# Optimization experiments

Hardware: AMD Instinct MI355X
Metric: run time of the kernel (lower is better)

The kernel has to match this reference:

```python
import jax, jax.numpy as jnp
import numpy as np

C_M, C_Z, H, C = 256, 128, 8, 32  # msa emb, pair emb, heads, head channels
S, R = 128, 256                   # MSA rows, residues


def layer_norm(x, gamma, beta, eps=1e-5):
    mu = jnp.mean(x, axis=-1, keepdims=True)
    var = jnp.var(x, axis=-1, keepdims=True)
    return (x - mu) * jax.lax.rsqrt(var + eps) * gamma + beta


def setup_inputs() -> dict:
    key = jax.random.key(0)
    ks = jax.random.split(key, 12)
    sc_m = 1.0 / np.sqrt(C_M)
    sc_z = 1.0 / np.sqrt(C_Z)
    sc_hc = 1.0 / np.sqrt(H * C)
    return {
        "msa_rep": jax.random.normal(ks[0], (S, R, C_M), dtype=jnp.float32),
        "pair_rep": jax.random.normal(ks[1], (R, R, C_Z), dtype=jnp.float32),
        "ln_msa_g": jnp.ones((C_M,), jnp.float32),
        "ln_msa_b": jnp.zeros((C_M,), jnp.float32),
        "ln_pair_g": jnp.ones((C_Z,), jnp.float32),
        "ln_pair_b": jnp.zeros((C_Z,), jnp.float32),
        "w_q": jax.random.normal(ks[2], (C_M, H, C), jnp.float32) * sc_m,
        "w_k": jax.random.normal(ks[3], (C_M, H, C), jnp.float32) * sc_m,
        "w_v": jax.random.normal(ks[4], (C_M, H, C), jnp.float32) * sc_m,
        "w_g": jax.random.normal(ks[5], (C_M, H, C), jnp.float32) * sc_m,
        "b_g": jnp.zeros((H, C), jnp.float32),
        "w_b": jax.random.normal(ks[6], (C_Z, H), jnp.float32) * sc_z,
        "b_b": jnp.zeros((H,), jnp.float32),
        "w_o": jax.random.normal(ks[7], (H, C, C_M), jnp.float32) * sc_hc,
        "b_o": jnp.zeros((C_M,), jnp.float32),
    }


def reference(msa_rep, pair_rep, ln_msa_g, ln_msa_b, ln_pair_g, ln_pair_b,
              w_q, w_k, w_v, w_g, b_g, w_b, b_b, w_o, b_o):
    m = layer_norm(msa_rep, ln_msa_g, ln_msa_b)                 # [S,R,C_M]
    q = jnp.einsum('src,chd->srhd', m, w_q)                     # [S,R,H,C]
    k = jnp.einsum('src,chd->srhd', m, w_k)
    v = jnp.einsum('src,chd->srhd', m, w_v)
    gates = jax.nn.sigmoid(jnp.einsum('src,chd->srhd', m, w_g) + b_g)
    # pair bias: [R,R,H] -> [H,R,R]
    z = layer_norm(pair_rep, ln_pair_g, ln_pair_b)
    b = jnp.einsum('ijc,ch->hij', z, w_b) + b_b[:, None, None]  # [H,R,R]
    logits = jnp.einsum('sqhd,skhd->shqk', q, k) / np.sqrt(C)   # [S,H,R,R]
    logits = logits + b[None]
    w = jax.nn.softmax(logits, axis=-1)
    o = jnp.einsum('shqk,skhd->sqhd', w, v)                     # [S,R,H,C]
    o = gates * o
    out = jnp.einsum('srhd,hdc->src', o, w_o) + b_o             # [S,R,C_M]
    return out
```

## Files before the change

### kernel.cpp

```cpp
#include <hip/hip_runtime.h>
#include <hip/hip_bf16.h>

#define S_DIM 128
#define R_DIM 256
#define CM 256
#define CZ 128
#define H_DIM 8
#define C_DIM 32

typedef short bf16x8 __attribute__((ext_vector_type(8)));
typedef float f32x4 __attribute__((ext_vector_type(4)));

__device__ inline ushort f2b(float f) {
  __hip_bfloat16 b = __float2bfloat16(f);
  return *(ushort*)&b;
}
__device__ inline float b2f(ushort u) {
  __hip_bfloat16 b = *(__hip_bfloat16*)&u;
  return __bfloat162float(b);
}

#define LOG2E 1.4426950408889634f

__device__ __forceinline__ void gld_lds16(const ushort* g, ushort* l) {
  __builtin_amdgcn_global_load_lds(
      (const __attribute__((address_space(1))) unsigned int*)g,
      (__attribute__((address_space(3))) unsigned int*)l, 16, 0, 0);
}

__global__ __launch_bounds__(256) void prologue_kernel(
    const float* __restrict__ msa, const float* __restrict__ ln_msa_g,
    const float* __restrict__ ln_msa_b, ushort* __restrict__ m,
    const float* __restrict__ pair, const float* __restrict__ ln_pr_g,
    const float* __restrict__ ln_pr_b, const float* __restrict__ w_b,
    const float* __restrict__ b_b, float* __restrict__ bias,
    const float* __restrict__ wq, const float* __restrict__ wk,
    const float* __restrict__ wv, const float* __restrict__ wg,
    const float* __restrict__ wo, ushort* __restrict__ Wt5) {
  __shared__ float t[64][65];
  __shared__ float wbs[CZ][8];
  __shared__ float gs[CZ], bs[CZ];
  int b = blockIdx.x;
  int tid = threadIdx.x;
  if (b < 8192) {
    int lane = tid & 63, w = tid >> 6;
    int row = b * 4 + w;
    const float* xp = msa + (size_t)row * CM + lane * 4;
    float4 v = *(const float4*)xp;
    float s1 = v.x + v.y + v.z + v.w;
    float s2 = v.x * v.x + v.y * v.y + v.z * v.z + v.w * v.w;
#pragma unroll
    for (int off = 32; off; off >>= 1) {
      s1 += __shfl_xor(s1, off, 64);
      s2 += __shfl_xor(s2, off, 64);
    }
    float mean = s1 * (1.0f / CM);
    float rstd = rsqrtf(s2 * (1.0f / CM) - mean * mean + 1e-5f);
    float4 gv = *(const float4*)(ln_msa_g + lane * 4);
    float4 bv = *(const float4*)(ln_msa_b + lane * 4);
    ushort4 o;
    o.x = f2b((v.x - mean) * rstd * gv.x + bv.x);
    o.y = f2b((v.y - mean) * rstd * gv.y + bv.y);
    o.z = f2b((v.z - mean) * rstd * gv.z + bv.z);
    o.w = f2b((v.w - mean) * rstd * gv.w + bv.w);
    *(ushort4*)(m + (size_t)row * CM + lane * 4) = o;
  } else if (b < 9216) {
    int bb = b - 8192;
    if (tid < CZ) { gs[tid] = ln_pr_g[tid]; bs[tid] = ln_pr_b[tid]; }
    for (int i = tid; i < CZ * 8; i += 256) wbs[i >> 3][i & 7] = w_b[i];
    __syncthreads();
    int q = tid & 3;
    int row = bb * 64 + (tid >> 2);
    const float* zp = pair + (size_t)row * CZ + q * 32;
    float4 v[8];
#pragma unroll
    for (int j = 0; j < 8; ++j) v[j] = *(const float4*)(zp + j * 4);
    float s1 = 0.f, s2 = 0.f;
#pragma unroll
    for (int j = 0; j < 8; ++j) {
      s1 += v[j].x + v[j].y + v[j].z + v[j].w;
      s2 += v[j].x * v[j].x + v[j].y * v[j].y + v[j].z * v[j].z +
            v[j].w * v[j].w;
    }
    s1 += __shfl_xor(s1, 1, 64);
    s2 += __shfl_xor(s2, 1, 64);
    s1 += __shfl_xor(s1, 2, 64);
    s2 += __shfl_xor(s2, 2, 64);
    float mean = s1 * (1.0f / CZ);
    float var = s2 * (1.0f / CZ) - mean * mean;
    float rstd = rsqrtf(var + 1e-5f);
    float acc[8] = {};
#pragma unroll
    for (int j = 0; j < 8; ++j) {
      float e[4] = {v[j].x, v[j].y, v[j].z, v[j].w};
#pragma unroll
      for (int u = 0; u < 4; ++u) {
        int c = q * 32 + j * 4 + u;
        float zn = (e[u] - mean) * rstd * gs[c] + bs[c];
#pragma unroll
        for (int h = 0; h < 8; ++h) acc[h] += zn * wbs[c][h];
      }
    }
#pragma unroll
    for (int h = 0; h < 8; ++h) {
      acc[h] += __shfl_xor(acc[h], 1, 64);
      acc[h] += __shfl_xor(acc[h], 2, 64);
    }
    int h0 = q * 2;
    bias[(size_t)h0 * (R_DIM * R_DIM) + row] = (acc[h0] + b_b[h0]) * LOG2E;
    bias[(size_t)(h0 + 1) * (R_DIM * R_DIM) + row] =
        (acc[h0 + 1] + b_b[h0 + 1]) * LOG2E;
  } else {
    int zz = b - 9216;
    int z = zz >> 4, rem = zz & 15;
    int by = rem >> 2, bx = rem & 3;
    const float* W = (z == 0) ? wq : (z == 1) ? wk : (z == 2) ? wv
                     : (z == 3) ? wg : wo;
    ushort* Wt = Wt5 + (size_t)z * 65536;
    int r = tid >> 2, c4 = (tid & 3) * 16;
    int rowBase = by * 64, colBase = bx * 64;
#pragma unroll
    for (int j = 0; j < 16; ++j)
      t[r][c4 + j] = W[(size_t)(rowBase + r) * 256 + colBase + c4 + j];
    __syncthreads();
#pragma unroll
    for (int j = 0; j < 16; ++j)
      Wt[(size_t)(colBase + r) * 256 + rowBase + c4 + j] = f2b(t[c4 + j][r]);
  }
}

__global__ __launch_bounds__(512) void proj_mfma(
    const ushort* __restrict__ M, const ushort* __restrict__ Wt5,
    const float* __restrict__ b_g, ushort* __restrict__ qb,
    ushort* __restrict__ kb2, ushort* __restrict__ vb,
    ushort* __restrict__ gb) {
  __shared__ ushort As[128 * 64];
  __shared__ ushort Bs[128 * 64];
  int tid = threadIdx.x, lane = tid & 63, wid = tid >> 6;
  int lr = lane & 15, lg = lane >> 4;
  int rowBase = blockIdx.x * 128;
  int cby = blockIdx.y;
  int proj = cby >> 1;
  int sc = (lane & 7) ^ ((lane >> 3) & 7);
  const ushort* Ag =
      M + (size_t)(rowBase + wid * 8 + (lane >> 3)) * 256 + sc * 8;
  const ushort* Bg =
      Wt5 + (size_t)(cby * 128 + wid * 8 + (lane >> 3)) * 256 + sc * 8;
  int ldsrow = wid * 8 * 64;
  int wr = wid >> 2, wc = wid & 3;
  int sx = (lr & 7) * 8;
  f32x4 zf = {0.f, 0.f, 0.f, 0.f};
  f32x4 acc[4][2];
#pragma unroll
  for (int i = 0; i < 4; ++i)
#pragma unroll
    for (int j = 0; j < 2; ++j) acc[i][j] = zf;

  for (int kb = 0; kb < 4; ++kb) {
    if (kb) __syncthreads();
    gld_lds16(Ag + kb * 64, As + ldsrow);
    gld_lds16(Ag + kb * 64 + 64 * 256, As + 64 * 64 + ldsrow);
    gld_lds16(Bg + kb * 64, Bs + ldsrow);
    gld_lds16(Bg + kb * 64 + 64 * 256, Bs + 64 * 64 + ldsrow);
    __syncthreads();
#pragma unroll
    for (int kk = 0; kk < 2; ++kk) {
      bf16x8 a[4], b[2];
#pragma unroll
      for (int mf = 0; mf < 4; ++mf)
        a[mf] = *(const bf16x8*)&As[(wr * 64 + mf * 16 + lr) * 64 +
                                    ((kk * 32 + lg * 8) ^ sx)];
#pragma unroll
      for (int nf = 0; nf < 2; ++nf)
        b[nf] = *(const bf16x8*)&Bs[(wc * 32 + nf * 16 + lr) * 64 +
                                    ((kk * 32 + lg * 8) ^ sx)];
#pragma unroll
      for (int mf = 0; mf < 4; ++mf)
#pragma unroll
        for (int nf = 0; nf < 2; ++nf)
          acc[mf][nf] = __builtin_amdgcn_mfma_f32_16x16x32_bf16(
              b[nf], a[mf], acc[mf][nf], 0, 0, 0);
    }
  }
#pragma unroll
  for (int mf = 0; mf < 4; ++mf) {
    int row = rowBase + wr * 64 + mf * 16 + lr;
    int s = row >> 8, rr = row & 255;
#pragma unroll
    for (int nf = 0; nf < 2; ++nf) {
      int colL = (cby & 1) * 128 + wc * 32 + nf * 16 + lg * 4;
      int h = colL >> 5, d0 = colL & 31;
      size_t oidx = ((size_t)((s * H_DIM + h) * R_DIM + rr)) * C_DIM + d0;
      f32x4 v4 = acc[mf][nf];
      ushort4 o4;
      if (proj == 0) {
        const float qs = 0.17677669529663687f * LOG2E;
        o4.x = f2b(v4[0] * qs);
        o4.y = f2b(v4[1] * qs);
        o4.z = f2b(v4[2] * qs);
        o4.w = f2b(v4[3] * qs);
        *(ushort4*)(qb + oidx) = o4;
      } else if (proj == 1) {
        o4.x = f2b(v4[0]); o4.y = f2b(v4[1]);
        o4.z = f2b(v4[2]); o4.w = f2b(v4[3]);
        *(ushort4*)(kb2 + oidx) = o4;
      } else if (proj == 2) {
        o4.x = f2b(v4[0]); o4.y = f2b(v4[1]);
        o4.z = f2b(v4[2]); o4.w = f2b(v4[3]);
        *(ushort4*)(vb + oidx) = o4;
      } else {
        float4 bg4 = *(const float4*)(b_g + colL);
        o4.x = f2b(1.f / (1.f + __expf(-(v4[0] + bg4.x))));
        o4.y = f2b(1.f / (1.f + __expf(-(v4[1] + bg4.y))));
        o4.z = f2b(1.f / (1.f + __expf(-(v4[2] + bg4.z))));
        o4.w = f2b(1.f / (1.f + __expf(-(v4[3] + bg4.w))));
        *(ushort4*)(gb + oidx) = o4;
      }
    }
  }
}

__global__ __launch_bounds__(512, 4) void attn_mfma(
    const ushort* __restrict__ q, const ushort* __restrict__ k,
    const ushort* __restrict__ v, const ushort* __restrict__ g,
    const float* __restrict__ bias, ushort* __restrict__ ob) {
  __shared__ ushort Vt[32][260];
  __shared__ ushort Pl[8][32][66];
  int blk = blockIdx.x;
  int s = blk >> 3, h = blk & 7;
  int tid = threadIdx.x, lane = tid & 63, w = tid >> 6;
  int lr = lane & 15, lg = lane >> 4;
  size_t base = (size_t)(s * H_DIM + h) * (R_DIM * C_DIM);

  {
    int key = tid >> 1, half = (tid & 1) * 16;
    const ushort* vp = v + base + (size_t)key * 32 + half;
    bf16x8 t0 = *(const bf16x8*)vp;
    bf16x8 t1 = *(const bf16x8*)(vp + 8);
#pragma unroll
    for (int j = 0; j < 8; ++j) {
      Vt[half + j][key] = (ushort)t0[j];
      Vt[half + 8 + j][key] = (ushort)t1[j];
    }
  }
  __syncthreads();

  int qrow0 = w * 32;
  bf16x8 qf[2];
#pragma unroll
  for (int mf = 0; mf < 2; ++mf)
    qf[mf] = *(const bf16x8*)(q + base + (size_t)(qrow0 + mf * 16 + lr) * 32 +
                              lg * 8);
  const float* bp0 = bias + ((size_t)h * R_DIM + qrow0 + lg * 4) * R_DIM +
                     lr * 4;

  float lsum[2][4] = {};
  f32x4 of[2][2];
  f32x4 zf = {0.f, 0.f, 0.f, 0.f};
#pragma unroll
  for (int mf = 0; mf < 2; ++mf) {
    of[mf][0] = zf;
    of[mf][1] = zf;
  }

  bf16x8 kf[4];
#pragma unroll
  for (int nf = 0; nf < 4; ++nf)
    kf[nf] = *(const bf16x8*)(k + base + (size_t)(lr * 4 + nf) * 32 + lg * 8);

#pragma unroll
  for (int t = 0; t < 4; ++t) {
    int k0 = t * 64;
    bf16x8 kfn[4];
    if (t < 3) {
#pragma unroll
      for (int nf = 0; nf < 4; ++nf)
        kfn[nf] = *(const bf16x8*)(k + base +
                                   (size_t)(k0 + 64 + lr * 4 + nf) * 32 +
                                   lg * 8);
    }
    f32x4 sf[2][4];
    __builtin_amdgcn_s_setprio(1);
#pragma unroll
    for (int mf = 0; mf < 2; ++mf)
#pragma unroll
      for (int nf = 0; nf < 4; ++nf)
        sf[mf][nf] =
            __builtin_amdgcn_mfma_f32_16x16x32_bf16(qf[mf], kf[nf], zf, 0, 0, 0);
    __builtin_amdgcn_s_setprio(0);
#pragma unroll
    for (int mf = 0; mf < 2; ++mf) {
      float4 bv[4];
#pragma unroll
      for (int r = 0; r < 4; ++r)
        bv[r] = *(const float4*)(bp0 + (size_t)(mf * 16 + r) * R_DIM + k0);
#pragma unroll
      for (int r = 0; r < 4; ++r) {
        float p0 = __builtin_amdgcn_exp2f(sf[mf][0][r] + bv[r].x);
        float p1 = __builtin_amdgcn_exp2f(sf[mf][1][r] + bv[r].y);
        float p2 = __builtin_amdgcn_exp2f(sf[mf][2][r] + bv[r].z);
        float p3 = __builtin_amdgcn_exp2f(sf[mf][3][r] + bv[r].w);
        lsum[mf][r] += (p0 + p1) + (p2 + p3);
        ushort4 pk;
        pk.x = f2b(p0);
        pk.y = f2b(p1);
        pk.z = f2b(p2);
        pk.w = f2b(p3);
        *(ushort4*)&Pl[w][mf * 16 + lg * 4 + r][lr * 4] = pk;
      }
    }
    __builtin_amdgcn_s_setprio(1);
#pragma unroll
    for (int kt = 0; kt < 2; ++kt) {
      bf16x8 pf[2], vf[2];
#pragma unroll
      for (int mf = 0; mf < 2; ++mf)
        pf[mf] = *(const bf16x8*)&Pl[w][mf * 16 + lr][kt * 32 + lg * 8];
#pragma unroll
      for (int df = 0; df < 2; ++df)
        vf[df] = *(const bf16x8*)&Vt[df * 16 + lr][k0 + kt * 32 + lg * 8];
#pragma unroll
      for (int mf = 0; mf < 2; ++mf)
#pragma unroll
        for (int df = 0; df < 2; ++df)
          of[mf][df] = __builtin_amdgcn_mfma_f32_16x16x32_bf16(
              vf[df], pf[mf], of[mf][df], 0, 0, 0);
    }
    __builtin_amdgcn_s_setprio(0);
    if (t < 3) {
#pragma unroll
      for (int nf = 0; nf < 4; ++nf) kf[nf] = kfn[nf];
    }
  }
#pragma unroll
  for (int mf = 0; mf < 2; ++mf)
#pragma unroll
    for (int r = 0; r < 4; ++r) {
#pragma unroll
      for (int msk = 1; msk <= 8; msk <<= 1)
        lsum[mf][r] += __shfl_xor(lsum[mf][r], msk, 64);
    }
  int srcl = ((lr >> 2) << 4) + lr;
  float invr[2];
#pragma unroll
  for (int mf = 0; mf < 2; ++mf) {
    float t0 = __shfl(lsum[mf][0], srcl, 64);
    float t1 = __shfl(lsum[mf][1], srcl, 64);
    float t2 = __shfl(lsum[mf][2], srcl, 64);
    float t3 = __shfl(lsum[mf][3], srcl, 64);
    int rb = lr & 3;
    float lv = rb == 0 ? t0 : rb == 1 ? t1 : rb == 2 ? t2 : t3;
    invr[mf] = 1.f / lv;
  }
#pragma unroll
  for (int mf = 0; mf < 2; ++mf) {
    int row = qrow0 + mf * 16 + lr;
#pragma unroll
    for (int df = 0; df < 2; ++df) {
      int d0 = df * 16 + lg * 4;
      ushort4 g4 = *(const ushort4*)(g + base + (size_t)row * 32 + d0);
      ushort4 o4;
      o4.x = f2b(of[mf][df][0] * invr[mf] * b2f(g4.x));
      o4.y = f2b(of[mf][df][1] * invr[mf] * b2f(g4.y));
      o4.z = f2b(of[mf][df][2] * invr[mf] * b2f(g4.z));
      o4.w = f2b(of[mf][df][3] * invr[mf] * b2f(g4.w));
      *(ushort4*)(ob + ((size_t)(s * R_DIM + row)) * 256 + h * 32 + d0) = o4;
    }
  }
}

__global__ __launch_bounds__(512) void out_mfma(
    const ushort* __restrict__ A, const ushort* __restrict__ Wt,
    const float* __restrict__ b_o, float* __restrict__ out) {
  __shared__ ushort As[128 * 64];
  __shared__ ushort Bs[128 * 64];
  int tid = threadIdx.x, lane = tid & 63, wid = tid >> 6;
  int lr = lane & 15, lg = lane >> 4;
  int rowBase = blockIdx.x * 128;
  int colBase = blockIdx.y * 128;
  int sc = (lane & 7) ^ ((lane >> 3) & 7);
  const ushort* Ag =
      A + (size_t)(rowBase + wid * 8 + (lane >> 3)) * 256 + sc * 8;
  const ushort* Bg =
      Wt + (size_t)(colBase + wid * 8 + (lane >> 3)) * 256 + sc * 8;
  int ldsrow = wid * 8 * 64;
  int wr = wid >> 2, wc = wid & 3;
  int sx = (lr & 7) * 8;
  f32x4 zf = {0.f, 0.f, 0.f, 0.f};
  f32x4 acc[4][2];
#pragma unroll
  for (int i = 0; i < 4; ++i)
#pragma unroll
    for (int j = 0; j < 2; ++j) acc[i][j] = zf;

  for (int kb = 0; kb < 4; ++kb) {
    if (kb) __syncthreads();
    gld_lds16(Ag + kb * 64, As + ldsrow);
    gld_lds16(Ag + kb * 64 + 64 * 256, As + 64 * 64 + ldsrow);
    gld_lds16(Bg + kb * 64, Bs + ldsrow);
    gld_lds16(Bg + kb * 64 + 64 * 256, Bs + 64 * 64 + ldsrow);
    __syncthreads();
#pragma unroll
    for (int kk = 0; kk < 2; ++kk) {
      bf16x8 a[4], b[2];
#pragma unroll
      for (int mf = 0; mf < 4; ++mf)
        a[mf] = *(const bf16x8*)&As[(wr * 64 + mf * 16 + lr) * 64 +
                                    ((kk * 32 + lg * 8) ^ sx)];
#pragma unroll
      for (int nf = 0; nf < 2; ++nf)
        b[nf] = *(const bf16x8*)&Bs[(wc * 32 + nf * 16 + lr) * 64 +
                                    ((kk * 32 + lg * 8) ^ sx)];
#pragma unroll
      for (int mf = 0; mf < 4; ++mf)
#pragma unroll
        for (int nf = 0; nf < 2; ++nf)
          acc[mf][nf] = __builtin_amdgcn_mfma_f32_16x16x32_bf16(
              b[nf], a[mf], acc[mf][nf], 0, 0, 0);
    }
  }
#pragma unroll
  for (int mf = 0; mf < 4; ++mf) {
    int row = rowBase + wr * 64 + mf * 16 + lr;
#pragma unroll
    for (int nf = 0; nf < 2; ++nf) {
      int col0 = colBase + wc * 32 + nf * 16 + lg * 4;
      float4 bo4 = *(const float4*)(b_o + col0);
      float4 o4;
      o4.x = acc[mf][nf][0] + bo4.x;
      o4.y = acc[mf][nf][1] + bo4.y;
      o4.z = acc[mf][nf][2] + bo4.z;
      o4.w = acc[mf][nf][3] + bo4.w;
      *(float4*)(out + (size_t)row * 256 + col0) = o4;
    }
  }
}

extern "C" void kernel_launch(void* const* d_in, const int* in_sizes, int n_in,
                              void* d_out, int out_size, void* d_ws,
                              size_t ws_size, hipStream_t stream) {
  const float* msa      = (const float*)d_in[0];
  const float* pair     = (const float*)d_in[1];
  const float* ln_msa_g = (const float*)d_in[2];
  const float* ln_msa_b = (const float*)d_in[3];
  const float* ln_pr_g  = (const float*)d_in[4];
  const float* ln_pr_b  = (const float*)d_in[5];
  const float* w_q      = (const float*)d_in[6];
  const float* w_k      = (const float*)d_in[7];
  const float* w_v      = (const float*)d_in[8];
  const float* w_g      = (const float*)d_in[9];
  const float* b_g      = (const float*)d_in[10];
  const float* w_b      = (const float*)d_in[11];
  const float* b_b      = (const float*)d_in[12];
  const float* w_o      = (const float*)d_in[13];
  const float* b_o      = (const float*)d_in[14];
  float* out = (float*)d_out;

  char* ws = (char*)d_ws;
  ushort* m   = (ushort*)(ws + 0);
  ushort* qb  = (ushort*)(ws + 16777216ull);
  ushort* kb  = (ushort*)(ws + 33554432ull);
  ushort* vb  = (ushort*)(ws + 50331648ull);
  ushort* gb  = (ushort*)(ws + 67108864ull);
  float*  bi  = (float*) (ws + 83886080ull);
  ushort* ob  = (ushort*)(ws + 85983232ull);
  ushort* Wt5 = (ushort*)(ws + 102760448ull);

  prologue_kernel<<<9296, 256, 0, stream>>>(
      msa, ln_msa_g, ln_msa_b, m, pair, ln_pr_g, ln_pr_b, w_b, b_b, bi,
      w_q, w_k, w_v, w_g, w_o, Wt5);
  proj_mfma<<<dim3(256, 8), 512, 0, stream>>>(m, Wt5, b_g, qb, kb, vb, gb);
  attn_mfma<<<S_DIM * H_DIM, 512, 0, stream>>>(qb, kb, vb, gb, bi, ob);
  out_mfma<<<dim3(256, 2), 512, 0, stream>>>(ob, Wt5 + 4 * 65536, b_o, out);
}
```

Measured before the change: 115.4 us.

## Process attention query fragments one at a time to halve P staging LDS

Restructures the per-tile loop so each 16-row query fragment runs score MFMA, exp/bias, LDS staging and PV MFMA before the next fragment starts. The per-wave P buffer in shared memory shrinks to half its size and fewer score accumulators are live at once, which lowers LDS use and register pressure and may allow more blocks per CU. In exchange, V fragments are reloaded from LDS for each query fragment and there is less independent MFMA work to interleave within each phase.

```diff
diff --git a/kernel.cpp b/kernel.cpp
--- a/kernel.cpp
+++ b/kernel.cpp
@@ -225,7 +225,7 @@
     const ushort* __restrict__ v, const ushort* __restrict__ g,
     const float* __restrict__ bias, ushort* __restrict__ ob) {
   __shared__ ushort Vt[32][260];
-  __shared__ ushort Pl[8][32][66];
+  __shared__ ushort Pl[8][16][66];
   int blk = blockIdx.x;
   int s = blk >> 3, h = blk & 7;
   int tid = threadIdx.x, lane = tid & 63, w = tid >> 6;
@@ -279,54 +279,46 @@
                                    (size_t)(k0 + 64 + lr * 4 + nf) * 32 +
                                    lg * 8);
     }
-    f32x4 sf[2][4];
-    __builtin_amdgcn_s_setprio(1);
-#pragma unroll
-    for (int mf = 0; mf < 2; ++mf)
+#pragma unroll
+    for (int mf = 0; mf < 2; ++mf) {
+      f32x4 sf[4];
+      __builtin_amdgcn_s_setprio(1);
 #pragma unroll
       for (int nf = 0; nf < 4; ++nf)
-        sf[mf][nf] =
+        sf[nf] =
             __builtin_amdgcn_mfma_f32_16x16x32_bf16(qf[mf], kf[nf], zf, 0, 0, 0);
-    __builtin_amdgcn_s_setprio(0);
-#pragma unroll
-    for (int mf = 0; mf < 2; ++mf) {
+      __builtin_amdgcn_s_setprio(0);
       float4 bv[4];
 #pragma unroll
       for (int r = 0; r < 4; ++r)
         bv[r] = *(const float4*)(bp0 + (size_t)(mf * 16 + r) * R_DIM + k0);
 #pragma unroll
       for (int r = 0; r < 4; ++r) {
-        float p0 = __builtin_amdgcn_exp2f(sf[mf][0][r] + bv[r].x);
-        float p1 = __builtin_amdgcn_exp2f(sf[mf][1][r] + bv[r].y);
-        float p2 = __builtin_amdgcn_exp2f(sf[mf][2][r] + bv[r].z);
-        float p3 = __builtin_amdgcn_exp2f(sf[mf][3][r] + bv[r].w);
+        float p0 = __builtin_amdgcn_exp2f(sf[0][r] + bv[r].x);
+        float p1 = __builtin_amdgcn_exp2f(sf[1][r] + bv[r].y);
+        float p2 = __builtin_amdgcn_exp2f(sf[2][r] + bv[r].z);
+        float p3 = __builtin_amdgcn_exp2f(sf[3][r] + bv[r].w);
         lsum[mf][r] += (p0 + p1) + (p2 + p3);
         ushort4 pk;
         pk.x = f2b(p0);
         pk.y = f2b(p1);
         pk.z = f2b(p2);
         pk.w = f2b(p3);
-        *(ushort4*)&Pl[w][mf * 16 + lg * 4 + r][lr * 4] = pk;
+        *(ushort4*)&Pl[w][lg * 4 + r][lr * 4] = pk;
       }
-    }
-    __builtin_amdgcn_s_setprio(1);
-#pragma unroll
-    for (int kt = 0; kt < 2; ++kt) {
-      bf16x8 pf[2], vf[2];
-#pragma unroll
-      for (int mf = 0; mf < 2; ++mf)
-        pf[mf] = *(const bf16x8*)&Pl[w][mf * 16 + lr][kt * 32 + lg * 8];
-#pragma unroll
-      for (int df = 0; df < 2; ++df)
-        vf[df] = *(const bf16x8*)&Vt[df * 16 + lr][k0 + kt * 32 + lg * 8];
-#pragma unroll
-      for (int mf = 0; mf < 2; ++mf)
-#pragma unroll
-        for (int df = 0; df < 2; ++df)
-          of[mf][df] = __builtin_amdgcn_mfma_f32_16x16x32_bf16(
-              vf[df], pf[mf], of[mf][df], 0, 0, 0);
-    }
-    __builtin_amdgcn_s_setprio(0);
+      __builtin_amdgcn_s_setprio(1);
+#pragma unroll
+      for (int kt = 0; kt < 2; ++kt) {
+        bf16x8 pf = *(const bf16x8*)&Pl[w][lr][kt * 32 + lg * 8];
+        bf16x8 vf0 = *(const bf16x8*)&Vt[lr][k0 + kt * 32 + lg * 8];
+        bf16x8 vf1 = *(const bf16x8*)&Vt[16 + lr][k0 + kt * 32 + lg * 8];
+        of[mf][0] = __builtin_amdgcn_mfma_f32_16x16x32_bf16(
+            vf0, pf, of[mf][0], 0, 0, 0);
+        of[mf][1] = __builtin_amdgcn_mfma_f32_16x16x32_bf16(
+            vf1, pf, of[mf][1], 0, 0, 0);
+      }
+      __builtin_amdgcn_s_setprio(0);
+    }
     if (t < 3) {
 #pragma unroll
       for (int nf = 0; nf < 4; ++nf) kf[nf] = kfn[nf];
```

Measured after the change: 116.3 us. Within noise of the previous version (+0.8%).
